# Performance work log

Measured on AMD Instinct MI355X. Metric: run time of the kernel, lower is better.

## Reference

```python
import jax, jax.numpy as jnp
import numpy as np

N_HEAD = 16
T_THRESHOLD = 0.001


def setup_inputs() -> dict:
    key = jax.random.key(0)
    k_x, k_wa, k_ba, k_wp, k_bp = jax.random.split(key, 5)
    B, P, L, R = 8, 1024, 4, 256
    C = L * R  # n_embd = 1024
    s = 1.0 / np.sqrt(C)
    return {
        "x": jax.random.normal(k_x, (B, P, L, R), dtype=jnp.float32),
        "w_attn": jax.random.normal(k_wa, (C, 3 * C), dtype=jnp.float32) * s,
        "b_attn": jax.random.normal(k_ba, (3 * C,), dtype=jnp.float32) * 0.01,
        "w_proj": jax.random.normal(k_wp, (C, C), dtype=jnp.float32) * s,
        "b_proj": jax.random.normal(k_bp, (C,), dtype=jnp.float32) * 0.01,
    }


def reference(x, w_attn, b_attn, w_proj, b_proj):
    B, P, L, R = x.shape
    C = L * R
    H = N_HEAD
    hd = C // H
    xf = x.reshape(B, P, C)                      # (B, T, C)
    qkv = xf @ w_attn + b_attn                   # (B, T, 3C)
    q, k, v = jnp.split(qkv, 3, axis=-1)
    # (B, H, T, hd)
    q = q.reshape(B, P, H, hd).transpose(0, 2, 1, 3)
    k = k.reshape(B, P, H, hd).transpose(0, 2, 1, 3)
    v = v.reshape(B, P, H, hd).transpose(0, 2, 1, 3)
    att = jnp.einsum("bhqd,bhkd->bhqk", q, k) * (1.0 / np.sqrt(hd))
    att = jax.nn.softmax(att, axis=-1)
    att = jax.nn.relu(att - T_THRESHOLD)         # post-softmax thresholding
    y = jnp.einsum("bhqk,bhkd->bhqd", att, v)    # (B, H, T, hd)
    y = y.transpose(0, 2, 1, 3).reshape(B, P, C)
    y = y @ w_proj + b_proj
    return y.reshape(B, P, L, R)
```

## Files before the change

kernel.cpp:

```cpp
#include <hip/hip_runtime.h>


typedef _Float16 half8 __attribute__((ext_vector_type(8)));
typedef _Float16 half4_t __attribute__((ext_vector_type(4)));
typedef float floatx4 __attribute__((ext_vector_type(4)));
typedef float floatx16 __attribute__((ext_vector_type(16)));
typedef unsigned int uint4v __attribute__((ext_vector_type(4)));

__device__ __forceinline__ void gl2lds16(const void* gsrc, void* lds) {
    __builtin_amdgcn_global_load_lds(
        (const __attribute__((address_space(1))) unsigned int*)gsrc,
        (__attribute__((address_space(3))) unsigned int*)lds,
        16, 0, 0);
}

__device__ __forceinline__ unsigned pkh(float a, float b) {
    _Float16 ha = (_Float16)a, hb = (_Float16)b;
    unsigned short ua = __builtin_bit_cast(unsigned short, ha);
    unsigned short ub = __builtin_bit_cast(unsigned short, hb);
    return (unsigned)ua | ((unsigned)ub << 16);
}

__global__ __launch_bounds__(256) void prep(const float4* __restrict__ x4,
                                            _Float16* __restrict__ xh,
                                            const float* __restrict__ wa,
                                            _Float16* __restrict__ waT,
                                            const float* __restrict__ wp,
                                            _Float16* __restrict__ wpT) {
    __shared__ _Float16 t[64 * 65];
    int bid = blockIdx.x;
    if (bid < 4096) {
        int idx = bid * 256 + threadIdx.x;
#pragma unroll
        for (int i = idx; i < 2097152; i += 1048576) {
            float4 v = x4[i];
            half4_t h = { (_Float16)v.x, (_Float16)v.y, (_Float16)v.z, (_Float16)v.w };
            *(half4_t*)(xh + (size_t)i * 4) = h;
        }
    } else {
        int tt = bid - 4096;
        int by = tt & 15, bx = tt >> 4;
        const float* in = wa; _Float16* out = waT; int C = 3072;
        if (bx >= 48) { bx -= 48; in = wp; out = wpT; C = 1024; }
#pragma unroll
        for (int it = 0; it < 16; ++it) {
            int idx = it * 256 + threadIdx.x;
            int r = idx >> 6, c = idx & 63;
            t[c * 65 + r] = (_Float16)in[(size_t)(by * 64 + r) * C + bx * 64 + c];
        }
        __syncthreads();
#pragma unroll
        for (int it = 0; it < 16; ++it) {
            int idx = it * 256 + threadIdx.x;
            int rn = idx >> 6, ck = idx & 63;
            out[(size_t)(bx * 64 + rn) * 1024 + by * 64 + ck] = t[rn * 65 + ck];
        }
    }
}

#define GBAR __builtin_amdgcn_s_barrier()
#define WLGKM do { asm volatile("s_waitcnt lgkmcnt(0)" ::: "memory"); } while (0)
#define WVM2  do { asm volatile("s_waitcnt vmcnt(2)"   ::: "memory"); } while (0)
#define WVM4  do { asm volatile("s_waitcnt vmcnt(4)"   ::: "memory"); } while (0)
#define WVM0  do { asm volatile("s_waitcnt vmcnt(0)"   ::: "memory"); } while (0)

#define WLDA(buf, rg)                                                                         \
    do {                                                                                      \
        _Pragma("unroll") for (int i = 0; i < 4; ++i) {                                       \
            int r_ = wm * 128 + ((rg) * 4 + i) * 16 + l15;                                    \
            _Pragma("unroll") for (int kk = 0; kk < 2; ++kk)                                  \
                a[i][kk] = *(const half8*)(sA + (buf) * 32768 + r_ * 128 +                    \
                                           ((((kk << 2) + quad) ^ (r_ & 7)) << 4));           \
        }                                                                                     \
    } while (0)

#define WLDB(buf, cg, bb)                                                                     \
    do {                                                                                      \
        _Pragma("unroll") for (int j = 0; j < 2; ++j) {                                       \
            int r_ = wn * 64 + ((cg) * 2 + j) * 16 + l15;                                     \
            _Pragma("unroll") for (int kk = 0; kk < 2; ++kk)                                  \
                bb[j][kk] = *(const half8*)(sB + (buf) * 32768 + r_ * 128 +                   \
                                            ((((kk << 2) + quad) ^ (r_ & 7)) << 4));          \
        }                                                                                     \
    } while (0)

#define WMMA(rg, cg, bb)                                                                      \
    do {                                                                                      \
        __builtin_amdgcn_s_setprio(1);                                                        \
        _Pragma("unroll") for (int kk = 0; kk < 2; ++kk)                                      \
            _Pragma("unroll") for (int i = 0; i < 4; ++i)                                     \
                _Pragma("unroll") for (int j = 0; j < 2; ++j)                                  \
                    acc[(rg) * 4 + i][(cg) * 2 + j] = __builtin_amdgcn_mfma_f32_16x16x32_f16( \
                        a[i][kk], bb[j][kk], acc[(rg) * 4 + i][(cg) * 2 + j], 0, 0, 0);       \
        __builtin_amdgcn_s_setprio(0);                                                        \
    } while (0)

__global__ __launch_bounds__(512, 2) void gemm_qkv(const _Float16* __restrict__ A,
                                                   const _Float16* __restrict__ BT,
                                                   const float* __restrict__ bias,
                                                   _Float16* __restrict__ qno,
                                                   _Float16* __restrict__ kPo,
                                                   _Float16* __restrict__ vPo) {
    __shared__ __attribute__((aligned(16))) char lds[131072];
    char* sA = lds;
    char* sB = lds + 65536;
    int tid = threadIdx.x;
    int W = tid >> 6, lane = tid & 63, quad = lane >> 4, l15 = lane & 15;
    int wm = W >> 2, wn = W & 3;
    int flat = blockIdx.y * 12 + blockIdx.x;
    int swz = (flat & 7) * 48 + (flat >> 3);
    int m0 = (swz / 12) * 256, n0 = (swz % 12) * 256;

    auto stA = [&](int buf, int half, int k0) {
#pragma unroll
        for (int rnd = 0; rnd < 2; ++rnd) {
            int c = rnd * 512 + tid;
            int row = c >> 3;
            int q = (c & 7) ^ (row & 7);
            const _Float16* src = A + (size_t)(m0 + half * 128 + row) * 1024 + k0 + q * 8;
            int off = __builtin_amdgcn_readfirstlane(buf * 32768 + half * 16384 +
                                                     rnd * 8192 + (W << 10));
            gl2lds16(src, sA + off);
        }
    };
    auto stB = [&](int buf, int half, int k0) {
#pragma unroll
        for (int rnd = 0; rnd < 2; ++rnd) {
            int c = rnd * 512 + tid;
            int row = c >> 3;
            int q = (c & 7) ^ (row & 7);
            const _Float16* src = BT + (size_t)(n0 + half * 128 + row) * 1024 + k0 + q * 8;
            int off = __builtin_amdgcn_readfirstlane(buf * 32768 + half * 16384 +
                                                     rnd * 8192 + (W << 10));
            gl2lds16(src, sB + off);
        }
    };

    half8 a[4][2], b0[2][2], b1[2][2];
    floatx4 acc[8][4] = {};

    stA(0, 0, 0); stA(0, 1, 0);
    stB(0, 0, 0); stB(0, 1, 0);
    stB(1, 0, 64); stB(1, 1, 64);
    WVM4;
    GBAR;

#pragma unroll 1
    for (int t = 0; t < 16; t += 2) {
        int k1 = (t + 1) << 6;
        int k2 = ((t + 2) & 15) << 6;
        int k3 = ((t + 3) & 15) << 6;
        WLDA(0, 0); WLDB(0, 0, b0); stA(1, 0, k1);
        GBAR; WLGKM; WMMA(0, 0, b0); GBAR;
        WLDB(0, 1, b1); stA(1, 1, k1);
        GBAR; WLGKM; WMMA(0, 1, b1); GBAR;
        WLDA(0, 1); stB(0, 0, k2);
        GBAR; WLGKM; WMMA(1, 1, b1); GBAR;
        stB(0, 1, k2); WVM4;
        GBAR; WLGKM; WMMA(1, 0, b0); GBAR;
        WLDA(1, 0); WLDB(1, 0, b0); stA(0, 0, k2);
        GBAR; WLGKM; WMMA(0, 0, b0); GBAR;
        WLDB(1, 1, b1); stA(0, 1, k2);
        GBAR; WLGKM; WMMA(0, 1, b1); GBAR;
        WLDA(1, 1); stB(1, 0, k3);
        GBAR; WLGKM; WMMA(1, 1, b1); GBAR;
        stB(1, 1, k3); WVM4;
        GBAR; WLGKM; WMMA(1, 0, b0); GBAR;
    }

    WVM0;
    GBAR;
    int sec = n0 >> 10;
    int b = m0 >> 10;
    int tb = m0 & 1023;
    int t31 = tid & 31, hi = (tid >> 5) & 1;
#pragma unroll 1
    for (int p = 0; p < 2; ++p) {
        if (p) __syncthreads();
        if (sec == 2) {
            if ((wn >> 1) == p) {
#pragma unroll
                for (int cf = 0; cf < 4; ++cf) {
                    int lc = (wn & 1) * 64 + cf * 16 + l15;
                    float bv = bias[n0 + wn * 64 + cf * 16 + l15];
#pragma unroll
                    for (int rf = 0; rf < 8; ++rf) {
                        int m = wm * 128 + rf * 16 + quad * 4;
                        half4_t h4;
#pragma unroll
                        for (int r = 0; r < 4; ++r) h4[r] = (_Float16)(acc[rf][cf][r] + bv);
                        *(half4_t*)(lds + lc * 528 + m * 2) = h4;
                    }
                }
            }
            __syncthreads();
            int nbV = (n0 & 1023) + p * 128;
#pragma unroll
            for (int i = 0; i < 8; ++i) {
                int g = W * 8 + i;
                int h_loc = g >> 5, dh = (g >> 4) & 1, kcl = g & 15;
                int lc = h_loc * 64 + dh * 32 + t31;
                half8 v = *(const half8*)(lds + lc * 528 + kcl * 32 + hi * 16);
                int hg = (nbV >> 6) + h_loc;
                size_t cv = ((size_t)((b * 16 + hg) * 64 + (tb >> 4) + kcl) * 2 + dh) * 64 + lane;
                *(half8*)(vPo + cv * 8) = v;
            }
        } else {
            if ((wn >> 1) == p) {
#pragma unroll
                for (int cf = 0; cf < 4; ++cf) {
                    int lc = (wn & 1) * 64 + cf * 16 + l15;
                    float bv = bias[n0 + wn * 64 + cf * 16 + l15];
#pragma unroll
                    for (int rf = 0; rf < 8; ++rf) {
                        int m = wm * 128 + rf * 16 + quad * 4;
#pragma unroll
                        for (int r = 0; r < 4; ++r)
                            *(_Float16*)(lds + (m + r) * 272 + lc * 2) =
                                (_Float16)(acc[rf][cf][r] + bv);
                    }
                }
            }
            __syncthreads();
            int nb = (n0 & 1023) + p * 128;
            if (sec == 0) {
                int noct = tid & 15;
#pragma unroll
                for (int i = 0; i < 8; ++i) {
                    int m = i * 32 + (tid >> 4);
                    half8 v = *(const half8*)(lds + m * 272 + (noct << 4));
                    *(half8*)(qno + (size_t)(b * 1024 + tb + m) * 1024 + nb + noct * 8) = v;
                }
            } else {
#pragma unroll
                for (int i = 0; i < 8; ++i) {
                    int g = W * 8 + i;
                    int h_loc = g >> 5, ks = (g >> 3) & 3, kbl = g & 7;
                    int m = kbl * 32 + t31;
                    int lc = h_loc * 64 + ks * 16 + hi * 8;
                    half8 v = *(const half8*)(lds + m * 272 + ((lc >> 3) << 4));
                    int hg = (nb >> 6) + h_loc;
                    size_t ck = ((size_t)((b * 16 + hg) * 32 + (tb >> 5) + kbl) * 4 + ks) * 64 + lane;
                    *(half8*)(kPo + ck * 8) = v;
                }
            }
        }
    }
}

#define LDA(buf, rg)                                                                          \
    do {                                                                                      \
        _Pragma("unroll") for (int i = 0; i < 2; ++i) {                                       \
            int r_ = wm * 64 + ((rg) * 2 + i) * 16 + l15;                                     \
            _Pragma("unroll") for (int kk = 0; kk < 2; ++kk)                                  \
                a[i][kk] = *(const half8*)(sA + (buf) * 32768 + r_ * 128 +                    \
                                           ((((kk << 2) + quad) ^ (r_ & 7)) << 4));           \
        }                                                                                     \
    } while (0)

#define LDB(buf, cg, bb)                                                                      \
    do {                                                                                      \
        _Pragma("unroll") for (int j = 0; j < 2; ++j) {                                       \
            int r_ = wn * 64 + ((cg) * 2 + j) * 16 + l15;                                     \
            _Pragma("unroll") for (int kk = 0; kk < 2; ++kk)                                  \
                bb[j][kk] = *(const half8*)(sB + (buf) * 16384 + r_ * 128 +                   \
                                            ((((kk << 2) + quad) ^ (r_ & 7)) << 4));          \
        }                                                                                     \
    } while (0)

#define MMA(rg, cg, bb)                                                                       \
    do {                                                                                      \
        __builtin_amdgcn_s_setprio(1);                                                        \
        _Pragma("unroll") for (int kk = 0; kk < 2; ++kk)                                      \
            _Pragma("unroll") for (int i = 0; i < 2; ++i)                                     \
                _Pragma("unroll") for (int j = 0; j < 2; ++j)                                  \
                    acc[(rg) * 2 + i][(cg) * 2 + j] = __builtin_amdgcn_mfma_f32_16x16x32_f16( \
                        a[i][kk], bb[j][kk], acc[(rg) * 2 + i][(cg) * 2 + j], 0, 0, 0);       \
        __builtin_amdgcn_s_setprio(0);                                                        \
    } while (0)

__global__ __launch_bounds__(512, 2) void gemm_proj(const _Float16* __restrict__ A,
                                                    const _Float16* __restrict__ BT,
                                                    const float* __restrict__ bias,
                                                    float* __restrict__ o0, int N) {
    __shared__ __attribute__((aligned(16))) char lds[98304];
    char* sA = lds;
    char* sB = lds + 65536;
    int tid = threadIdx.x;
    int W = tid >> 6, lane = tid & 63, quad = lane >> 4, l15 = lane & 15;
    int wm = W >> 1, wn = W & 1;
    int flat = blockIdx.y * 8 + blockIdx.x;
    int swz = (flat & 7) * 32 + (flat >> 3);
    int m0 = (swz >> 3) * 256, n0 = (swz & 7) * 128;

    auto stA = [&](int buf, int half, int k0) {
#pragma unroll
        for (int rnd = 0; rnd < 2; ++rnd) {
            int c = rnd * 512 + tid;
            int row = c >> 3;
            int q = (c & 7) ^ (row & 7);
            const _Float16* src = A + (size_t)(m0 + half * 128 + row) * 1024 + k0 + q * 8;
            int off = __builtin_amdgcn_readfirstlane(buf * 32768 + half * 16384 +
                                                     rnd * 8192 + (W << 10));
            gl2lds16(src, sA + off);
        }
    };
    auto stB = [&](int buf, int half, int k0) {
        int row = tid >> 3;
        int q = (tid & 7) ^ (row & 7);
        const _Float16* src = BT + (size_t)(n0 + half * 64 + row) * 1024 + k0 + q * 8;
        int off = __builtin_amdgcn_readfirstlane(buf * 16384 + half * 8192 + (W << 10));
        gl2lds16(src, sB + off);
    };

    half8 a[2][2], b0[2][2], b1[2][2];
    floatx4 acc[4][4] = {};

    stA(0, 0, 0); stA(0, 1, 0);
    stB(0, 0, 0); stB(0, 1, 0);
    stB(1, 0, 64); stB(1, 1, 64);
    WVM2;
    GBAR;

#pragma unroll 1
    for (int t = 0; t < 16; t += 2) {
        int k1 = (t + 1) << 6;
        int k2 = ((t + 2) & 15) << 6;
        int k3 = ((t + 3) & 15) << 6;
        LDA(0, 0); LDB(0, 0, b0); stA(1, 0, k1);
        GBAR; WLGKM; MMA(0, 0, b0); GBAR;
        LDB(0, 1, b1); stA(1, 1, k1);
        GBAR; WLGKM; MMA(0, 1, b1); GBAR;
        LDA(0, 1); stB(0, 0, k2);
        GBAR; WLGKM; MMA(1, 1, b1); GBAR;
        stB(0, 1, k2); WVM2;
        GBAR; WLGKM; MMA(1, 0, b0); GBAR;
        LDA(1, 0); LDB(1, 0, b0); stA(0, 0, k2);
        GBAR; WLGKM; MMA(0, 0, b0); GBAR;
        LDB(1, 1, b1); stA(0, 1, k2);
        GBAR; WLGKM; MMA(0, 1, b1); GBAR;
        LDA(1, 1); stB(1, 0, k3);
        GBAR; WLGKM; MMA(1, 1, b1); GBAR;
        stB(1, 1, k3); WVM2;
        GBAR; WLGKM; MMA(1, 0, b0); GBAR;
    }

#pragma unroll
    for (int cf = 0; cf < 4; ++cf) {
        int gn = n0 + wn * 64 + cf * 16 + l15;
        float bv = bias[gn];
#pragma unroll
        for (int rf = 0; rf < 4; ++rf) {
            int gmBase = m0 + wm * 64 + rf * 16 + quad * 4;
#pragma unroll
            for (int r = 0; r < 4; ++r)
                o0[(size_t)(gmBase + r) * N + gn] = acc[rf][cf][r] + bv;
        }
    }
}

__global__ __launch_bounds__(512, 4) void attn(const _Float16* __restrict__ qn,
                                               const _Float16* __restrict__ kP,
                                               const _Float16* __restrict__ vP,
                                               _Float16* __restrict__ y) {
    __shared__ __attribute__((aligned(16))) char red[65536];
    __shared__ float lsum[8][32];
    int tid = threadIdx.x;
    int W = tid >> 6, lane = tid & 63;
    int l31 = lane & 31, hi = lane >> 5;
    int flat = blockIdx.y * 32 + blockIdx.x;
    int swz = (flat & 7) * 512 + (flat >> 3);
    int qt = swz & 31, bh = swz >> 5;
    int b = bh >> 4, h = bh & 15;
    int q0 = qt * 32;

    half8 bq[4];
#pragma unroll
    for (int ks = 0; ks < 4; ++ks)
        bq[ks] = *(const half8*)(qn + (size_t)(b * 1024 + q0 + l31) * 1024 +
                                 h * 64 + ks * 16 + hi * 8);

    half8 pd[4][2];
    float lp0 = 0.f, lp1 = 0.f;
#pragma unroll
    for (int kb = 0; kb < 4; ++kb) {
        const _Float16* kpb = kP + ((size_t)((bh * 32 + W * 4 + kb) * 4) * 64 + lane) * 8;
        half8 ak0 = *(const half8*)(kpb);
        half8 ak1 = *(const half8*)(kpb + 512);
        half8 ak2 = *(const half8*)(kpb + 1024);
        half8 ak3 = *(const half8*)(kpb + 1536);
        floatx16 s = {};
        __builtin_amdgcn_s_setprio(1);
        s = __builtin_amdgcn_mfma_f32_32x32x16_f16(ak0, bq[0], s, 0, 0, 0);
        s = __builtin_amdgcn_mfma_f32_32x32x16_f16(ak1, bq[1], s, 0, 0, 0);
        s = __builtin_amdgcn_mfma_f32_32x32x16_f16(ak2, bq[2], s, 0, 0, 0);
        s = __builtin_amdgcn_mfma_f32_32x32x16_f16(ak3, bq[3], s, 0, 0, 0);
        __builtin_amdgcn_s_setprio(0);
        float e[16];
#pragma unroll
        for (int r = 0; r < 16; ++r)
            e[r] = __builtin_amdgcn_exp2f(fminf(s[r] * 0.18033688f, 14.4269504f));
        lp0 += ((e[0] + e[1]) + (e[2] + e[3])) + ((e[4] + e[5]) + (e[6] + e[7]));
        lp1 += ((e[8] + e[9]) + (e[10] + e[11])) + ((e[12] + e[13]) + (e[14] + e[15]));
#pragma unroll
        for (int c = 0; c < 2; ++c) {
            int o = c * 8;
            unsigned P01 = pkh(e[o + 0], e[o + 1]);
            unsigned P23 = pkh(e[o + 2], e[o + 3]);
            unsigned P45 = pkh(e[o + 4], e[o + 5]);
            unsigned P67 = pkh(e[o + 6], e[o + 7]);
            unsigned P01p = (unsigned)__shfl_xor((int)P45, 32);
            unsigned P45p = (unsigned)__shfl_xor((int)P01, 32);
            unsigned P23p = (unsigned)__shfl_xor((int)P67, 32);
            unsigned P67p = (unsigned)__shfl_xor((int)P23, 32);
            uint4v F;
            F[0] = hi ? P01p : P01;
            F[1] = hi ? P23p : P23;
            F[2] = hi ? P45 : P45p;
            F[3] = hi ? P67 : P67p;
            pd[kb][c] = __builtin_bit_cast(half8, F);
        }
    }
    {
        float lp = lp0 + lp1;
        lp += __shfl_xor(lp, 32);
        if (lane < 32) lsum[W][l31] = lp;
    }
    __syncthreads();

    half8 inv8, t8, z8;
#pragma unroll
    for (int j = 0; j < 8; ++j) { t8[j] = (_Float16)(-0.001f); z8[j] = (_Float16)0.f; }
    {
        float l = 0.f;
#pragma unroll
        for (int w = 0; w < 8; ++w) l += lsum[w][l31];
        _Float16 invh = (_Float16)(1.0f / l);
#pragma unroll
        for (int j = 0; j < 8; ++j) inv8[j] = invh;
    }
#pragma unroll
    for (int kb = 0; kb < 4; ++kb)
#pragma unroll
        for (int c = 0; c < 2; ++c) {
            pd[kb][c] = pd[kb][c] * inv8 + t8;
            pd[kb][c] = __builtin_elementwise_max(pd[kb][c], z8);
        }

    floatx16 acc[2] = {};
#pragma unroll
    for (int kb = 0; kb < 4; ++kb)
#pragma unroll
        for (int c = 0; c < 2; ++c) {
            int kc = (W * 4 + kb) * 2 + c;
            const _Float16* vpb = vP + ((size_t)((bh * 64 + kc) * 2) * 64 + lane) * 8;
            half8 bv0 = *(const half8*)(vpb);
            half8 bv1 = *(const half8*)(vpb + 512);
            __builtin_amdgcn_s_setprio(1);
            acc[0] = __builtin_amdgcn_mfma_f32_32x32x16_f16(pd[kb][c], bv0, acc[0], 0, 0, 0);
            acc[1] = __builtin_amdgcn_mfma_f32_32x32x16_f16(pd[kb][c], bv1, acc[1], 0, 0, 0);
            __builtin_amdgcn_s_setprio(0);
        }

#pragma unroll
    for (int dh = 0; dh < 2; ++dh)
#pragma unroll
        for (int r = 0; r < 16; ++r) {
            int q = (r & 3) + 8 * (r >> 2) + 4 * hi;
            *(float*)(red + q * 2048 + W * 256 + (dh * 32 + l31) * 4) = acc[dh][r];
        }
    __syncthreads();
    {
        int e4 = tid * 4;
        int r = e4 >> 6, c = e4 & 63;
        floatx4 s = {};
#pragma unroll
        for (int w = 0; w < 8; ++w)
            s += *(const floatx4*)(red + r * 2048 + w * 256 + c * 4);
        half4_t hv = { (_Float16)s[0], (_Float16)s[1], (_Float16)s[2], (_Float16)s[3] };
        *(half4_t*)(y + (size_t)(b * 1024 + q0 + r) * 1024 + h * 64 + c) = hv;
    }
}

extern "C" void kernel_launch(void* const* d_in, const int* in_sizes, int n_in,
                              void* d_out, int out_size, void* d_ws, size_t ws_size,
                              hipStream_t stream) {
    const float* x  = (const float*)d_in[0];
    const float* wa = (const float*)d_in[1];
    const float* ba = (const float*)d_in[2];
    const float* wp = (const float*)d_in[3];
    const float* bp = (const float*)d_in[4];
    float* out = (float*)d_out;

    char* ws = (char*)d_ws;
    _Float16* y   = (_Float16*)(ws);
    _Float16* qn  = (_Float16*)(ws + 16777216);
    _Float16* kP  = (_Float16*)(ws + 33554432);
    _Float16* vP  = (_Float16*)(ws + 50331648);
    _Float16* waT = (_Float16*)(ws + 67108864);
    _Float16* wpT = (_Float16*)(ws + 73400320);
    _Float16* xh  = (_Float16*)(ws + 75497472);

    prep<<<5120, 256, 0, stream>>>((const float4*)x, xh, wa, waT, wp, wpT);
    gemm_qkv<<<dim3(12, 32), 512, 0, stream>>>(xh, waT, ba, qn, kP, vP);
    attn<<<dim3(32, 128), 512, 0, stream>>>(qn, kP, vP, y);
    gemm_proj<<<dim3(8, 32), 512, 0, stream>>>(y, wpT, bp, out, 1024);
}
```

Measured before the change: 266.0 us.

## Rework K/V packed layouts for coalesced stores and use permlane32 swap in softmax

Changes the packed K and V fragment layouts written by the QKV GEMM epilogue so that stores come from contiguous LDS reads, and updates the attention kernel's address math to match. The shfl_xor and select sequence that redistributes P fragments is replaced with v_permlane32_swap_b32. The clamp before exp2 is removed. The intent is cheaper epilogue scatter and fewer cross-lane ops, but dropping the clamp risks fp16 overflow for large scores.

```diff
diff --git a/kernel.cpp b/kernel.cpp
--- a/kernel.cpp
+++ b/kernel.cpp
@@ -63,6 +63,7 @@
 #define WVM2  do { asm volatile("s_waitcnt vmcnt(2)"   ::: "memory"); } while (0)
 #define WVM4  do { asm volatile("s_waitcnt vmcnt(4)"   ::: "memory"); } while (0)
 #define WVM0  do { asm volatile("s_waitcnt vmcnt(0)"   ::: "memory"); } while (0)
+
 
 #define WLDA(buf, rg)                                                                         \
     do {                                                                                      \
@@ -173,7 +174,6 @@
     int sec = n0 >> 10;
     int b = m0 >> 10;
     int tb = m0 & 1023;
-    int t31 = tid & 31, hi = (tid >> 5) & 1;
 #pragma unroll 1
     for (int p = 0; p < 2; ++p) {
         if (p) __syncthreads();
@@ -194,16 +194,21 @@
                 }
             }
             __syncthreads();
+            int l15v = tid & 15;
+            int moct = W * 4 + ((tid >> 4) & 3);
+            int t = tb + moct * 8;
+            int kbv = (t >> 5) & 31, quad_v = (t >> 3) & 3;
             int nbV = (n0 & 1023) + p * 128;
 #pragma unroll
             for (int i = 0; i < 8; ++i) {
-                int g = W * 8 + i;
-                int h_loc = g >> 5, dh = (g >> 4) & 1, kcl = g & 15;
-                int lc = h_loc * 64 + dh * 32 + t31;
-                half8 v = *(const half8*)(lds + lc * 528 + kcl * 32 + hi * 16);
-                int hg = (nbV >> 6) + h_loc;
-                size_t cv = ((size_t)((b * 16 + hg) * 64 + (tb >> 4) + kcl) * 2 + dh) * 64 + lane;
-                *(half8*)(vPo + cv * 8) = v;
+                int hh = i >> 2, cf = i & 3;
+                int n = hh * 64 + cf * 16 + l15v;
+                half8 v = *(const half8*)(lds + n * 528 + (moct << 4));
+                int gcol = nbV + n;
+                int h = gcol >> 6, d = gcol & 63;
+                size_t chunk = (size_t)((b * 16 + h) * 32 + kbv) * 256 +
+                               (d >> 4) * 64 + quad_v * 16 + (d & 15);
+                *(half8*)(vPo + chunk * 8) = v;
             }
         } else {
             if ((wn >> 1) == p) {
@@ -232,16 +237,18 @@
                     *(half8*)(qno + (size_t)(b * 1024 + tb + m) * 1024 + nb + noct * 8) = v;
                 }
             } else {
+                int l15k = tid & 15, noct = (tid >> 4) & 15;
 #pragma unroll
                 for (int i = 0; i < 8; ++i) {
-                    int g = W * 8 + i;
-                    int h_loc = g >> 5, ks = (g >> 3) & 3, kbl = g & 7;
-                    int m = kbl * 32 + t31;
-                    int lc = h_loc * 64 + ks * 16 + hi * 8;
-                    half8 v = *(const half8*)(lds + m * 272 + ((lc >> 3) << 4));
-                    int hg = (nb >> 6) + h_loc;
-                    size_t ck = ((size_t)((b * 16 + hg) * 32 + (tb >> 5) + kbl) * 4 + ks) * 64 + lane;
-                    *(half8*)(kPo + ck * 8) = v;
+                    int mb = i * 2 + (tid >> 8);
+                    int m = mb * 16 + l15k;
+                    half8 v = *(const half8*)(lds + m * 272 + (noct << 4));
+                    int gcol = nb + noct * 8;
+                    int h = gcol >> 6, d0 = gcol & 63;
+                    int t = tb + m;
+                    size_t chunk = (size_t)((b * 16 + h) * 64 + (t >> 4)) * 128 +
+                                   (d0 >> 5) * 64 + ((d0 >> 3) & 3) * 16 + l15k;
+                    *(half8*)(kPo + chunk * 8) = v;
                 }
             }
         }
@@ -374,6 +381,9 @@
     int b = bh >> 4, h = bh & 15;
     int q0 = qt * 32;
 
+    const _Float16* kPb = kP + (size_t)bh * 8192 * 8;
+    const _Float16* vPb = vP + (size_t)bh * 8192 * 8;
+
     half8 bq[4];
 #pragma unroll
     for (int ks = 0; ks < 4; ++ks)
@@ -381,14 +391,14 @@
                                  h * 64 + ks * 16 + hi * 8);
 
     half8 pd[4][2];
-    float lp0 = 0.f, lp1 = 0.f;
+    float lpA = 0.f, lpB = 0.f;
 #pragma unroll
     for (int kb = 0; kb < 4; ++kb) {
-        const _Float16* kpb = kP + ((size_t)((bh * 32 + W * 4 + kb) * 4) * 64 + lane) * 8;
-        half8 ak0 = *(const half8*)(kpb);
-        half8 ak1 = *(const half8*)(kpb + 512);
-        half8 ak2 = *(const half8*)(kpb + 1024);
-        half8 ak3 = *(const half8*)(kpb + 1536);
+        int cbase = (W * 8 + kb * 2 + (l31 >> 4)) * 128 + (l31 & 15);
+        half8 ak0 = *(const half8*)(kPb + (size_t)(cbase + hi * 16) * 8);
+        half8 ak1 = *(const half8*)(kPb + (size_t)(cbase + (2 + hi) * 16) * 8);
+        half8 ak2 = *(const half8*)(kPb + (size_t)(cbase + 64 + hi * 16) * 8);
+        half8 ak3 = *(const half8*)(kPb + (size_t)(cbase + 64 + (2 + hi) * 16) * 8);
         floatx16 s = {};
         __builtin_amdgcn_s_setprio(1);
         s = __builtin_amdgcn_mfma_f32_32x32x16_f16(ak0, bq[0], s, 0, 0, 0);
@@ -399,30 +409,24 @@
         float e[16];
 #pragma unroll
         for (int r = 0; r < 16; ++r)
-            e[r] = __builtin_amdgcn_exp2f(fminf(s[r] * 0.18033688f, 14.4269504f));
-        lp0 += ((e[0] + e[1]) + (e[2] + e[3])) + ((e[4] + e[5]) + (e[6] + e[7]));
-        lp1 += ((e[8] + e[9]) + (e[10] + e[11])) + ((e[12] + e[13]) + (e[14] + e[15]));
-#pragma unroll
-        for (int c = 0; c < 2; ++c) {
-            int o = c * 8;
+            e[r] = __builtin_amdgcn_exp2f(s[r] * 0.18033688f);
+        lpA += ((e[0] + e[1]) + (e[2] + e[3])) + ((e[4] + e[5]) + (e[6] + e[7]));
+        lpB += ((e[8] + e[9]) + (e[10] + e[11])) + ((e[12] + e[13]) + (e[14] + e[15]));
+#pragma unroll
+        for (int c2 = 0; c2 < 2; ++c2) {
+            int o = c2 * 8;
             unsigned P01 = pkh(e[o + 0], e[o + 1]);
             unsigned P23 = pkh(e[o + 2], e[o + 3]);
             unsigned P45 = pkh(e[o + 4], e[o + 5]);
             unsigned P67 = pkh(e[o + 6], e[o + 7]);
-            unsigned P01p = (unsigned)__shfl_xor((int)P45, 32);
-            unsigned P45p = (unsigned)__shfl_xor((int)P01, 32);
-            unsigned P23p = (unsigned)__shfl_xor((int)P67, 32);
-            unsigned P67p = (unsigned)__shfl_xor((int)P23, 32);
-            uint4v F;
-            F[0] = hi ? P01p : P01;
-            F[1] = hi ? P23p : P23;
-            F[2] = hi ? P45 : P45p;
-            F[3] = hi ? P67 : P67p;
-            pd[kb][c] = __builtin_bit_cast(half8, F);
+            asm("v_permlane32_swap_b32 %0, %1" : "+v"(P01), "+v"(P45));
+            asm("v_permlane32_swap_b32 %0, %1" : "+v"(P23), "+v"(P67));
+            uint4v F = { P01, P23, P45, P67 };
+            pd[kb][c2] = __builtin_bit_cast(half8, F);
         }
     }
     {
-        float lp = lp0 + lp1;
+        float lp = lpA + lpB;
         lp += __shfl_xor(lp, 32);
         if (lane < 32) lsum[W][l31] = lp;
     }
@@ -442,33 +446,33 @@
 #pragma unroll
     for (int kb = 0; kb < 4; ++kb)
 #pragma unroll
-        for (int c = 0; c < 2; ++c) {
-            pd[kb][c] = pd[kb][c] * inv8 + t8;
-            pd[kb][c] = __builtin_elementwise_max(pd[kb][c], z8);
-        }
-
-    floatx16 acc[2] = {};
+        for (int c2 = 0; c2 < 2; ++c2) {
+            pd[kb][c2] = pd[kb][c2] * inv8 + t8;
+            pd[kb][c2] = __builtin_elementwise_max(pd[kb][c2], z8);
+        }
+
+    floatx16 acc0 = {}, acc1 = {};
 #pragma unroll
     for (int kb = 0; kb < 4; ++kb)
 #pragma unroll
-        for (int c = 0; c < 2; ++c) {
-            int kc = (W * 4 + kb) * 2 + c;
-            const _Float16* vpb = vP + ((size_t)((bh * 64 + kc) * 2) * 64 + lane) * 8;
-            half8 bv0 = *(const half8*)(vpb);
-            half8 bv1 = *(const half8*)(vpb + 512);
+        for (int c2 = 0; c2 < 2; ++c2) {
+            int kc = (W * 4 + kb) * 2 + c2;
+            int vbase = (kc >> 1) * 256 + (l31 >> 4) * 64 + ((kc & 1) * 2 + hi) * 16 +
+                        (l31 & 15);
+            half8 bv0 = *(const half8*)(vPb + (size_t)vbase * 8);
+            half8 bv1 = *(const half8*)(vPb + (size_t)(vbase + 128) * 8);
             __builtin_amdgcn_s_setprio(1);
-            acc[0] = __builtin_amdgcn_mfma_f32_32x32x16_f16(pd[kb][c], bv0, acc[0], 0, 0, 0);
-            acc[1] = __builtin_amdgcn_mfma_f32_32x32x16_f16(pd[kb][c], bv1, acc[1], 0, 0, 0);
+            acc0 = __builtin_amdgcn_mfma_f32_32x32x16_f16(pd[kb][c2], bv0, acc0, 0, 0, 0);
+            acc1 = __builtin_amdgcn_mfma_f32_32x32x16_f16(pd[kb][c2], bv1, acc1, 0, 0, 0);
             __builtin_amdgcn_s_setprio(0);
         }
 
 #pragma unroll
-    for (int dh = 0; dh < 2; ++dh)
-#pragma unroll
-        for (int r = 0; r < 16; ++r) {
-            int q = (r & 3) + 8 * (r >> 2) + 4 * hi;
-            *(float*)(red + q * 2048 + W * 256 + (dh * 32 + l31) * 4) = acc[dh][r];
-        }
+    for (int r = 0; r < 16; ++r) {
+        int q = (r & 3) + 8 * (r >> 2) + 4 * hi;
+        *(float*)(red + q * 2048 + W * 256 + l31 * 4) = acc0[r];
+        *(float*)(red + q * 2048 + W * 256 + 128 + l31 * 4) = acc1[r];
+    }
     __syncthreads();
     {
         int e4 = tid * 4;
```

After: 262.6 us. No clear change (-1.3%).
